# Optimization experiments

Hardware: AMD Instinct MI355X
Metric: run time of the kernel (lower is better)

Reference implementation:

```python
import jax, jax.numpy as jnp
import numpy as np

N = 50000
E = 600000
D = 128


def gcn_conv(x, row, col, w, W, b):
    """PyG GCNConv: add self-loops (weight 1), symmetric deg^-1/2 normalization,
    linear transform, edge-weighted scatter-add aggregation, then bias."""
    n = x.shape[0]
    loop = jnp.arange(n)
    r = jnp.concatenate([row, loop])            # source nodes, [E+N]
    c = jnp.concatenate([col, loop])            # target nodes, [E+N]
    ww = jnp.concatenate([w, jnp.ones((n,), x.dtype)])
    deg = jax.ops.segment_sum(ww, c, num_segments=n)          # weighted in-degree
    dinv = jnp.where(deg > 0, jax.lax.rsqrt(deg), jnp.zeros_like(deg))
    norm = dinv[r] * ww * dinv[c]               # [E+N]
    xl = x @ W                                  # [n, D_out]
    msg = norm[:, None] * xl[r]                 # gather + scale, [E+N, D_out]
    out = jax.ops.segment_sum(msg, c, num_segments=n)
    return out + b


def setup_inputs() -> dict:
    key = jax.random.key(0)
    ks = jax.random.split(key, 12)
    x = jax.random.normal(ks[0], (N, D), dtype=jnp.float32)
    edge_index = jax.random.randint(ks[1], (2, E), 0, N, dtype=jnp.int64)
    edge_weights = jax.random.uniform(ks[2], (E,), dtype=jnp.float32)
    s = 1.0 / np.sqrt(D)
    W1 = jax.random.uniform(ks[3], (D, D), jnp.float32, -s, s)
    b1 = jnp.zeros((D,), jnp.float32)
    W2 = jax.random.uniform(ks[4], (D, D), jnp.float32, -s, s)
    b2 = jnp.zeros((D,), jnp.float32)
    W3 = jax.random.uniform(ks[5], (D, D), jnp.float32, -s, s)
    b3 = jnp.zeros((D,), jnp.float32)
    prelu_w = jnp.array(0.25, jnp.float32)
    return {"x": x, "edge_index": edge_index, "edge_weights": edge_weights,
            "W1": W1, "b1": b1, "W2": W2, "b2": b2, "W3": W3, "b3": b3,
            "prelu_w": prelu_w}


def reference(x, edge_index, edge_weights, W1, b1, W2, b2, W3, b3, prelu_w):
    row, col = edge_index[0], edge_index[1]
    # layer 1: GCNConv -> (dropout: eval, identity) -> ELU
    h = gcn_conv(x, row, col, edge_weights, W1, b1)
    h = jax.nn.elu(h)
    # layer 2: GCNConv -> GELU (torch default = exact erf)
    h = gcn_conv(h, row, col, edge_weights, W2, b2)
    h = jax.nn.gelu(h, approximate=False)
    # layer 3: GCNConv -> PReLU (learnable scalar slope)
    h = gcn_conv(h, row, col, edge_weights, W3, b3)
    h = jnp.where(h >= 0, h, prelu_w * h)
    return h
```

## Files before the change

kernel.cpp:

```cpp
#include <hip/hip_runtime.h>
#include <hip/hip_fp16.h>
#include <math.h>

constexpr int D = 128;
constexpr int CAPF = 512;

struct __align__(16) H8 { __half2 h[4]; };

typedef _Float16     half8   __attribute__((ext_vector_type(8)));
typedef float        floatx4 __attribute__((ext_vector_type(4)));
typedef unsigned int uint4v  __attribute__((ext_vector_type(4)));
typedef unsigned int uint2v  __attribute__((ext_vector_type(2)));


__device__ __forceinline__ int detect64(const int* __restrict__ ei) {
  int z = 0;
#pragma unroll
  for (int i = 0; i < 8; ++i) z |= ei[2 * i + 1];
  return (z == 0) ? 1 : 0;
}

__device__ __forceinline__ void load_edge(const int* __restrict__ ei, int e, int nE,
                                          int m64, int n, int& r, int& c) {
  if (m64) { r = ei[2 * (size_t)e]; c = ei[2 * ((size_t)nE + e)]; }
  else     { r = ei[(size_t)e];     c = ei[(size_t)nE + e]; }
  r = min(max(r, 0), n - 1);
  c = min(max(c, 0), n - 1);
}

__global__ void k_setup(const float* __restrict__ W1, const float* __restrict__ W2,
                        const float* __restrict__ W3, __half* __restrict__ Wt,
                        unsigned long long* __restrict__ cntdeg, int n8) {
  int b = blockIdx.x;
  if (b < 24) {
    int m = b >> 3, s = b & 7;
    const float* W = m == 0 ? W1 : (m == 1 ? W2 : W3);
    __half* o = Wt + (size_t)m * D * D;
    int t = threadIdx.x;
    int nn = t & 127;
    int kh = t >> 7;
    int k0 = s * 16 + kh * 8;
    H8 hv;
#pragma unroll
    for (int jj = 0; jj < 4; ++jj) {
      float f0 = W[(size_t)(k0 + 2 * jj)     * D + nn];
      float f1 = W[(size_t)(k0 + 2 * jj + 1) * D + nn];
      hv.h[jj] = __floats2half2_rn(f0, f1);
    }
    *(H8*)(o + (size_t)nn * D + k0) = hv;
  } else {
    int i = (b - 24) * 256 + threadIdx.x;
    if (i < n8) cntdeg[i] = 0ULL;
  }
}

template <int ACT>
__device__ __forceinline__ float act_f(float x) {
  if (ACT == 1) return x > 0.f ? x : expm1f(x);
  if (ACT == 2) return 0.5f * x * (1.0f + erff(x * 0.70710678118654752440f));
  return x;
}

__device__ __forceinline__ void gemm_body(int bid, const float* __restrict__ A,
                                          const __half* __restrict__ Wt,
                                          __half* __restrict__ Y, int n) {
  const int wave = threadIdx.x >> 6;
  const int lane = threadIdx.x & 63;
  const int np = lane & 15;
  const int quad = lane >> 4;
  const int node = bid * 64 + wave * 16 + np;
  const int nc = min(node, n - 1);

  half8 b[4];
#pragma unroll
  for (int s = 0; s < 4; ++s) {
    const float* ap = A + (size_t)nc * D + s * 32 + quad * 8;
    floatx4 v0 = __builtin_nontemporal_load((const floatx4*)ap);
    floatx4 v1 = __builtin_nontemporal_load((const floatx4*)(ap + 4));
#pragma unroll
    for (int t = 0; t < 4; ++t) {
      b[s][t]     = (_Float16)v0[t];
      b[s][t + 4] = (_Float16)v1[t];
    }
  }

  floatx4 acc[8];
#pragma unroll
  for (int mt = 0; mt < 8; ++mt) acc[mt] = (floatx4){0.f, 0.f, 0.f, 0.f};

#pragma unroll
  for (int mt = 0; mt < 8; ++mt) {
#pragma unroll
    for (int s = 0; s < 4; ++s) {
      half8 a = *(const half8*)(Wt + (size_t)(mt * 16 + np) * D + s * 32 + quad * 8);
      acc[mt] = __builtin_amdgcn_mfma_f32_16x16x32_f16(a, b[s], acc[mt], 0, 0, 0);
    }
  }

  if (node < n) {
#pragma unroll
    for (int mt = 0; mt < 8; ++mt) {
      __half2 ha = __floats2half2_rn(acc[mt][0], acc[mt][1]);
      __half2 hb = __floats2half2_rn(acc[mt][2], acc[mt][3]);
      uint2v pv;
      pv[0] = *(unsigned int*)&ha;
      pv[1] = *(unsigned int*)&hb;
      int f0 = mt * 16 + quad * 4;
      __builtin_nontemporal_store(
          pv, (uint2v*)(Y + ((size_t)(f0 >> 5) * n + node) * 32 + (f0 & 31)));
    }
  }
}

__global__ __launch_bounds__(256) void k_posgemm(const float* __restrict__ x,
                                                 const __half* __restrict__ Wt,
                                                 __half* __restrict__ Y,
                                                 const int* __restrict__ ei,
                                                 const float* __restrict__ w,
                                                 unsigned long long* __restrict__ cntdeg,
                                                 int2* __restrict__ rc,
                                                 int* __restrict__ pos,
                                                 int nE, int n, int gb) {
  int b = blockIdx.x;
  if (b < gb) {
    gemm_body(b, x, Wt, Y, n);
    return;
  }
  int e = (b - gb) * blockDim.x + threadIdx.x;
  if (e >= nE) return;
  int m64 = detect64(ei);
  int r, c;
  load_edge(ei, e, nE, m64, n, r, c);
  rc[e] = make_int2(r, c);
  float wf = fminf(fmaxf(w[e], 0.0f), 65535.0f);
  unsigned long long pk =
      (1ULL << 32) | (unsigned long long)__float2uint_rn(wf * 65536.0f);
  unsigned long long old = atomicAdd(&cntdeg[(size_t)c << 3], pk);
  pos[e] = (int)(old >> 32);
}

__global__ void k_scan1(const unsigned long long* __restrict__ cntdeg,
                        int* __restrict__ offs, int* __restrict__ bsum, int n) {
  __shared__ int s[256];
  int t = threadIdx.x;
  int i = blockIdx.x * 256 + t;
  int v = 0;
  if (i < n) {
    int cn = (int)(cntdeg[(size_t)i << 3] >> 32);
    v = (cn + 3) & ~3;
  }
  s[t] = v;
  __syncthreads();
  for (int off = 1; off < 256; off <<= 1) {
    int x = 0;
    if (t >= off) x = s[t - off];
    __syncthreads();
    if (t >= off) s[t] += x;
    __syncthreads();
  }
  if (i < n) offs[i] = s[t] - v;
  if (t == 255) bsum[blockIdx.x] = s[255];
}

__global__ void k_scan23(int* __restrict__ offs, const int* __restrict__ bsum,
                         const unsigned long long* __restrict__ cntdeg,
                         float* __restrict__ dinv, int n, int nb) {
  __shared__ int s[256];
  int t = threadIdx.x;
  int v = (t < nb) ? bsum[t] : 0;
  s[t] = v;
  __syncthreads();
  for (int off = 1; off < 256; off <<= 1) {
    int x = 0;
    if (t >= off) x = s[t - off];
    __syncthreads();
    if (t >= off) s[t] += x;
    __syncthreads();
  }
  int b = blockIdx.x;
  int boffb = (b == 0) ? 0 : s[b - 1];
  int i = b * 256 + t;
  if (i < n) {
    offs[i] += boffb;
    float degf =
        (float)(unsigned int)(cntdeg[(size_t)i << 3] & 0xffffffffULL) * (1.0f / 65536.0f);
    dinv[i] = rsqrtf(1.0f + degf);
  }
  if (i == 0) offs[n] = s[nb - 1];
}

__global__ void k_fill(const int2* __restrict__ rc, const int* __restrict__ pos,
                       const float* __restrict__ w, const int* __restrict__ offs,
                       const unsigned long long* __restrict__ cntdeg,
                       const float* __restrict__ dinv,
                       unsigned int* __restrict__ ecf2, int nE, int n) {
  int e = blockIdx.x * blockDim.x + threadIdx.x;
  if (e < nE) {
    int2 p = rc[e];
    int idx = offs[p.y] + pos[e];
    float cf = dinv[p.x] * w[e];
    ecf2[idx] = ((unsigned int)p.x << 16) |
                (unsigned int)__half_as_ushort(__float2half_rn(cf));
  }
  if (e < n) {
    int q0 = offs[e] + (int)(cntdeg[(size_t)e << 3] >> 32), q1 = offs[e + 1];
    for (int q = q0; q < q1; ++q) ecf2[q] = 0;
  }
}

__device__ __forceinline__ void fmacc8(float* acc, float c, const H8& y) {
  const _Float16* hp = (const _Float16*)&y;
#pragma unroll
  for (int i = 0; i < 8; ++i) acc[i] = fmaf(c, (float)hp[i], acc[i]);
}

__device__ __forceinline__ float cdecode(unsigned int u) {
  return __half2float(__ushort_as_half((unsigned short)(u & 0xffffu)));
}

__device__ __forceinline__ void gather4(H8* y, uint4v u, const __half* __restrict__ Yc,
                                        int j) {
#pragma unroll
  for (int i = 0; i < 4; ++i)
    y[i] = *(const H8*)(Yc + (size_t)(u[i] >> 16) * 32 + j * 8);
}

__device__ __forceinline__ void accum4(float* acc, uint4v u, const H8* y) {
#pragma unroll
  for (int i = 0; i < 4; ++i) fmacc8(acc, cdecode(u[i]), y[i]);
}

#define AGG_PHASE()                                                              \
  const int nl = t >> 4;                                                         \
  const int node = node0 + nl;                                                   \
  const int cj = t & 15;                                                         \
  const int chunk = cj >> 2, j = cj & 3;                                         \
  const __half* Yc = Yin + (size_t)chunk * n * 32;                               \
  const int ncl = min(node, n - 1);                                              \
  float dc = dinv[ncl];                                                          \
  float acc[8] = {0.f, 0.f, 0.f, 0.f, 0.f, 0.f, 0.f, 0.f};                       \
  H8 ys = *(const H8*)(Yc + (size_t)ncl * 32 + j * 8);                           \
  {                                                                              \
    int lo = soff[nl], hi = soff[nl + 1];                                        \
    for (int b = lo; b < hi; b += 8) {                                           \
      bool has2 = (hi - b) > 4;                                                  \
      int k0 = b - seg_lo;                                                       \
      uint4v u0 = (k0 + 4 <= CAPF) ? *(const uint4v*)&sc[k0]                     \
                                   : *(const uint4v*)(ecf2 + b);                 \
      uint4v u1{};                                                               \
      if (has2) {                                                                \
        int k1 = k0 + 4;                                                         \
        u1 = (k1 + 4 <= CAPF) ? *(const uint4v*)&sc[k1]                          \
                              : *(const uint4v*)(ecf2 + b + 4);                  \
      }                                                                          \
      H8 y0[4], y1[4];                                                           \
      gather4(y0, u0, Yc, j);                                                    \
      if (has2) gather4(y1, u1, Yc, j);                                          \
      accum4(acc, u0, y0);                                                       \
      if (has2) accum4(acc, u1, y1);                                             \
    }                                                                            \
    fmacc8(acc, dc, ys);                                                         \
  }

#define STAGE_COEFS()                                                            \
  const int t = threadIdx.x;                                                     \
  const int node0 = blockIdx.x * 16;                                             \
  if (node0 >= n) return;                                                        \
  const int seg_lo = offs[node0];                                                \
  const int seg_hi = offs[min(node0 + 16, n)];                                   \
  const int segN = min(seg_hi - seg_lo, CAPF);                                   \
  for (int i = t * 4; i < segN; i += 1024)                                       \
    *(uint4v*)&sc[i] =                                                           \
        __builtin_nontemporal_load((const uint4v*)(ecf2 + seg_lo + i));          \
  if (t < 17) soff[t] = offs[min(node0 + t, n)];                                 \
  __syncthreads();

template <int ACT>
__global__ __launch_bounds__(256, 6) void k_aggemm(
    const __half* __restrict__ Yin, const int* __restrict__ offs,
    const unsigned int* __restrict__ ecf2, const float* __restrict__ dinv,
    const float* __restrict__ bias, const __half* __restrict__ Wt,
    __half* __restrict__ Yout, int n) {
  __shared__ unsigned int sc[CAPF];
  __shared__ __half ht[16 * 136];
  __shared__ int soff[17];
  STAGE_COEFS();
  {
    AGG_PHASE();
    floatx4 ba = *(const floatx4*)(bias + chunk * 32 + j * 8);
    floatx4 bb = *(const floatx4*)(bias + chunk * 32 + j * 8 + 4);
    float o[8];
#pragma unroll
    for (int i = 0; i < 8; ++i)
      o[i] = act_f<ACT>(dc * acc[i] + (i < 4 ? ba[i] : bb[i - 4]));
    H8 hw;
#pragma unroll
    for (int i = 0; i < 4; ++i) hw.h[i] = __floats2half2_rn(o[2 * i], o[2 * i + 1]);
    if (node < n) *(H8*)&ht[nl * 136 + chunk * 32 + j * 8] = hw;
  }
  __syncthreads();

  const int wave = t >> 6, lane = t & 63, np = lane & 15, quad = lane >> 4;
  half8 bfr[4];
#pragma unroll
  for (int s = 0; s < 4; ++s)
    bfr[s] = *(const half8*)&ht[np * 136 + s * 32 + quad * 8];
  floatx4 ga0 = (floatx4){0.f, 0.f, 0.f, 0.f};
  floatx4 ga1 = (floatx4){0.f, 0.f, 0.f, 0.f};
#pragma unroll
  for (int s = 0; s < 4; ++s) {
    half8 a0 = *(const half8*)(Wt + (size_t)((wave * 2) * 16 + np) * D + s * 32 + quad * 8);
    ga0 = __builtin_amdgcn_mfma_f32_16x16x32_f16(a0, bfr[s], ga0, 0, 0, 0);
    half8 a1 = *(const half8*)(Wt + (size_t)((wave * 2 + 1) * 16 + np) * D + s * 32 + quad * 8);
    ga1 = __builtin_amdgcn_mfma_f32_16x16x32_f16(a1, bfr[s], ga1, 0, 0, 0);
  }
  const int gnode = node0 + np;
  if (gnode < n) {
    floatx4 g[2] = {ga0, ga1};
#pragma unroll
    for (int mi = 0; mi < 2; ++mi) {
      int mt = wave * 2 + mi;
      __half2 ha = __floats2half2_rn(g[mi][0], g[mi][1]);
      __half2 hb = __floats2half2_rn(g[mi][2], g[mi][3]);
      uint2v pv;
      pv[0] = *(unsigned int*)&ha;
      pv[1] = *(unsigned int*)&hb;
      int f0 = mt * 16 + quad * 4;
      __builtin_nontemporal_store(
          pv, (uint2v*)(Yout + ((size_t)(f0 >> 5) * n + gnode) * 32 + (f0 & 31)));
    }
  }
}

__global__ __launch_bounds__(256, 6) void k_aggout(
    const __half* __restrict__ Yin, const int* __restrict__ offs,
    const unsigned int* __restrict__ ecf2, const float* __restrict__ dinv,
    const float* __restrict__ bias, const float* __restrict__ pw,
    float* __restrict__ out, int n) {
  __shared__ unsigned int sc[CAPF];
  __shared__ int soff[17];
  STAGE_COEFS();
  AGG_PHASE();
  if (node < n) {
    floatx4 ba = *(const floatx4*)(bias + chunk * 32 + j * 8);
    floatx4 bb = *(const floatx4*)(bias + chunk * 32 + j * 8 + 4);
    float wv = *pw;
    floatx4 v0, v1;
#pragma unroll
    for (int i = 0; i < 4; ++i) {
      float o = dc * acc[i] + ba[i];
      v0[i] = o >= 0.f ? o : wv * o;
    }
#pragma unroll
    for (int i = 0; i < 4; ++i) {
      float o = dc * acc[4 + i] + bb[i];
      v1[i] = o >= 0.f ? o : wv * o;
    }
    float* op = out + (size_t)node * D + chunk * 32 + j * 8;
    __builtin_nontemporal_store(v0, (floatx4*)op);
    __builtin_nontemporal_store(v1, (floatx4*)(op + 4));
  }
}

extern "C" void kernel_launch(void* const* d_in, const int* in_sizes, int n_in,
                              void* d_out, int out_size, void* d_ws, size_t ws_size,
                              hipStream_t stream) {
  const float* x  = (const float*)d_in[0];
  const int*   ei = (const int*)d_in[1];
  const float* w  = (const float*)d_in[2];
  const float* W1 = (const float*)d_in[3];
  const float* b1 = (const float*)d_in[4];
  const float* W2 = (const float*)d_in[5];
  const float* b2 = (const float*)d_in[6];
  const float* W3 = (const float*)d_in[7];
  const float* b3 = (const float*)d_in[8];
  const float* pw = (const float*)d_in[9];
  const int N = in_sizes[0] / D;
  const int E = in_sizes[2];
  float* out = (float*)d_out;

  char* wsb = (char*)d_ws;
  size_t off = 0;
  auto alloc = [&](size_t bytes) {
    void* p = wsb + off;
    off = (off + bytes + 255) & ~(size_t)255;
    return p;
  };
  float*              dinv   = (float*)alloc((size_t)N * 4);
  unsigned long long* cntdeg = (unsigned long long*)alloc((size_t)N * 64);
  int*                offs   = (int*)alloc((size_t)(N + 1) * 4);
  int*                bsum   = (int*)alloc(256 * 4);
  unsigned int*       ecf2   = (unsigned int*)alloc(((size_t)E + 3 * (size_t)N + 64) * 4);
  __half*             Wt     = (__half*)alloc((size_t)3 * D * D * 2);
  __half*             Ya     = (__half*)alloc((size_t)N * D * 2);
  __half*             Yb     = (__half*)alloc((size_t)N * D * 2);
  int2*               rc     = (int2*)alloc((size_t)E * 8);
  int*                pos    = (int*)alloc((size_t)E * 4);

  const int nbN = (N + 255) / 256;
  const int eb  = (E + 255) / 256;
  const int fb  = ((E > N ? E : N) + 255) / 256;
  const int n8  = N * 8;
  const int zb  = (n8 + 255) / 256;
  const int gb  = (N + 63) / 64;
  const int abf = (N + 15) / 16;

  hipLaunchKernelGGL(k_setup,   dim3(24 + zb), dim3(256), 0, stream, W1, W2, W3, Wt, cntdeg, n8);
  hipLaunchKernelGGL(k_posgemm, dim3(gb + eb), dim3(256), 0, stream, x, Wt, Ya, ei, w, cntdeg,
                     rc, pos, E, N, gb);
  hipLaunchKernelGGL(k_scan1,   dim3(nbN), dim3(256), 0, stream, cntdeg, offs, bsum, N);
  hipLaunchKernelGGL(k_scan23,  dim3(nbN), dim3(256), 0, stream, offs, bsum, cntdeg, dinv, N, nbN);
  hipLaunchKernelGGL(k_fill,    dim3(fb),  dim3(256), 0, stream, rc, pos, w, offs, cntdeg, dinv, ecf2, E, N);

  hipLaunchKernelGGL((k_aggemm<1>), dim3(abf), dim3(256), 0, stream, Ya, offs, ecf2, dinv, b1, Wt + D * D,     Yb, N);
  hipLaunchKernelGGL((k_aggemm<2>), dim3(abf), dim3(256), 0, stream, Yb, offs, ecf2, dinv, b2, Wt + 2 * D * D, Ya, N);
  hipLaunchKernelGGL(k_aggout,      dim3(abf), dim3(256), 0, stream, Ya, offs, ecf2, dinv, b3, pw, out, N);
}
```

Measured before the change: 289.4 us.

## Split fused aggregate-GEMM into chunk-major aggregation and separate half GEMM kernels

```diff
diff --git a/kernel.cpp b/kernel.cpp
--- a/kernel.cpp
+++ b/kernel.cpp
@@ -3,7 +3,7 @@
 #include <math.h>
 
 constexpr int D = 128;
-constexpr int CAPF = 512;
+constexpr int CAPS = 2048;
 
 struct __align__(16) H8 { __half2 h[4]; };
 
@@ -83,6 +83,50 @@
       b[s][t + 4] = (_Float16)v1[t];
     }
   }
+
+  floatx4 acc[8];
+#pragma unroll
+  for (int mt = 0; mt < 8; ++mt) acc[mt] = (floatx4){0.f, 0.f, 0.f, 0.f};
+
+#pragma unroll
+  for (int mt = 0; mt < 8; ++mt) {
+#pragma unroll
+    for (int s = 0; s < 4; ++s) {
+      half8 a = *(const half8*)(Wt + (size_t)(mt * 16 + np) * D + s * 32 + quad * 8);
+      acc[mt] = __builtin_amdgcn_mfma_f32_16x16x32_f16(a, b[s], acc[mt], 0, 0, 0);
+    }
+  }
+
+  if (node < n) {
+#pragma unroll
+    for (int mt = 0; mt < 8; ++mt) {
+      __half2 ha = __floats2half2_rn(acc[mt][0], acc[mt][1]);
+      __half2 hb = __floats2half2_rn(acc[mt][2], acc[mt][3]);
+      uint2v pv;
+      pv[0] = *(unsigned int*)&ha;
+      pv[1] = *(unsigned int*)&hb;
+      int f0 = mt * 16 + quad * 4;
+      __builtin_nontemporal_store(
+          pv, (uint2v*)(Y + ((size_t)(f0 >> 5) * n + node) * 32 + (f0 & 31)));
+    }
+  }
+}
+
+__global__ __launch_bounds__(256) void k_gemmh(const __half* __restrict__ A,
+                                               const __half* __restrict__ Wt,
+                                               __half* __restrict__ Y, int n) {
+  const int wave = threadIdx.x >> 6;
+  const int lane = threadIdx.x & 63;
+  const int np = lane & 15;
+  const int quad = lane >> 4;
+  const int node = blockIdx.x * 64 + wave * 16 + np;
+  const int nc = min(node, n - 1);
+
+  half8 b[4];
+#pragma unroll
+  for (int s = 0; s < 4; ++s)
+    b[s] = __builtin_nontemporal_load(
+        (const half8*)(A + ((size_t)s * n + nc) * 32 + quad * 8));
 
   floatx4 acc[8];
 #pragma unroll
@@ -230,135 +274,87 @@
   for (int i = 0; i < 4; ++i) fmacc8(acc, cdecode(u[i]), y[i]);
 }
 
-#define AGG_PHASE()                                                              \
-  const int nl = t >> 4;                                                         \
-  const int node = node0 + nl;                                                   \
-  const int cj = t & 15;                                                         \
-  const int chunk = cj >> 2, j = cj & 3;                                         \
-  const __half* Yc = Yin + (size_t)chunk * n * 32;                               \
-  const int ncl = min(node, n - 1);                                              \
-  float dc = dinv[ncl];                                                          \
-  float acc[8] = {0.f, 0.f, 0.f, 0.f, 0.f, 0.f, 0.f, 0.f};                       \
-  H8 ys = *(const H8*)(Yc + (size_t)ncl * 32 + j * 8);                           \
-  {                                                                              \
-    int lo = soff[nl], hi = soff[nl + 1];                                        \
-    for (int b = lo; b < hi; b += 8) {                                           \
-      bool has2 = (hi - b) > 4;                                                  \
-      int k0 = b - seg_lo;                                                       \
-      uint4v u0 = (k0 + 4 <= CAPF) ? *(const uint4v*)&sc[k0]                     \
-                                   : *(const uint4v*)(ecf2 + b);                 \
-      uint4v u1{};                                                               \
-      if (has2) {                                                                \
-        int k1 = k0 + 4;                                                         \
-        u1 = (k1 + 4 <= CAPF) ? *(const uint4v*)&sc[k1]                          \
-                              : *(const uint4v*)(ecf2 + b + 4);                  \
-      }                                                                          \
-      H8 y0[4], y1[4];                                                           \
-      gather4(y0, u0, Yc, j);                                                    \
-      if (has2) gather4(y1, u1, Yc, j);                                          \
-      accum4(acc, u0, y0);                                                       \
-      if (has2) accum4(acc, u1, y1);                                             \
-    }                                                                            \
-    fmacc8(acc, dc, ys);                                                         \
-  }
-
-#define STAGE_COEFS()                                                            \
-  const int t = threadIdx.x;                                                     \
-  const int node0 = blockIdx.x * 16;                                             \
-  if (node0 >= n) return;                                                        \
-  const int seg_lo = offs[node0];                                                \
-  const int seg_hi = offs[min(node0 + 16, n)];                                   \
-  const int segN = min(seg_hi - seg_lo, CAPF);                                   \
-  for (int i = t * 4; i < segN; i += 1024)                                       \
-    *(uint4v*)&sc[i] =                                                           \
-        __builtin_nontemporal_load((const uint4v*)(ecf2 + seg_lo + i));          \
-  if (t < 17) soff[t] = offs[min(node0 + t, n)];                                 \
+template <int ACT, int PRELU, typename OutT>
+__global__ __launch_bounds__(256) void k_agg(const __half* __restrict__ Yin,
+                                             const int* __restrict__ offs,
+                                             const unsigned int* __restrict__ ecf2,
+                                             const float* __restrict__ dinv,
+                                             const float* __restrict__ bias,
+                                             const float* __restrict__ pw,
+                                             OutT* __restrict__ OUT, int n) {
+  __shared__ unsigned int sc[CAPS];
+  __shared__ int soff[65];
+  const int chunk = blockIdx.x & 3;
+  const int t = threadIdx.x;
+  const int node0 = (blockIdx.x >> 2) * 64;
+  const int nl = t >> 2;
+  const int node = node0 + nl;
+  const int j = t & 3;
+
+  const int seg_lo = offs[node0];
+  const int seg_hi = offs[min(node0 + 64, n)];
+  const int segN = min(seg_hi - seg_lo, CAPS);
+  for (int i = t * 4; i < segN; i += 1024)
+    *(uint4v*)&sc[i] =
+        __builtin_nontemporal_load((const uint4v*)(ecf2 + seg_lo + i));
+  if (t < 65) soff[t] = offs[min(node0 + t, n)];
   __syncthreads();
 
-template <int ACT>
-__global__ __launch_bounds__(256, 6) void k_aggemm(
-    const __half* __restrict__ Yin, const int* __restrict__ offs,
-    const unsigned int* __restrict__ ecf2, const float* __restrict__ dinv,
-    const float* __restrict__ bias, const __half* __restrict__ Wt,
-    __half* __restrict__ Yout, int n) {
-  __shared__ unsigned int sc[CAPF];
-  __shared__ __half ht[16 * 136];
-  __shared__ int soff[17];
-  STAGE_COEFS();
-  {
-    AGG_PHASE();
+  const __half* Yc = Yin + (size_t)chunk * n * 32;
+  const int ncl = min(node, n - 1);
+  float dc = dinv[ncl];
+  float acc[8] = {0.f, 0.f, 0.f, 0.f, 0.f, 0.f, 0.f, 0.f};
+
+  H8 ys = *(const H8*)(Yc + (size_t)ncl * 32 + j * 8);
+
+  int lo = soff[nl], hi = soff[nl + 1];
+  if (lo < hi) {
+    int k = lo - seg_lo;
+    uint4v uc = (k + 4 <= CAPS) ? *(const uint4v*)&sc[k]
+                                : *(const uint4v*)(ecf2 + lo);
+    H8 yc[4];
+    gather4(yc, uc, Yc, j);
+    for (int b = lo + 4; b < hi; b += 4) {
+      int k2 = b - seg_lo;
+      uint4v un = (k2 + 4 <= CAPS) ? *(const uint4v*)&sc[k2]
+                                   : *(const uint4v*)(ecf2 + b);
+      H8 yn[4];
+      gather4(yn, un, Yc, j);
+      accum4(acc, uc, yc);
+      uc = un;
+#pragma unroll
+      for (int q = 0; q < 4; ++q) yc[q] = yn[q];
+    }
+    accum4(acc, uc, yc);
+  }
+  fmacc8(acc, dc, ys);
+
+  if (node < n) {
     floatx4 ba = *(const floatx4*)(bias + chunk * 32 + j * 8);
     floatx4 bb = *(const floatx4*)(bias + chunk * 32 + j * 8 + 4);
     float o[8];
 #pragma unroll
     for (int i = 0; i < 8; ++i)
       o[i] = act_f<ACT>(dc * acc[i] + (i < 4 ? ba[i] : bb[i - 4]));
-    H8 hw;
-#pragma unroll
-    for (int i = 0; i < 4; ++i) hw.h[i] = __floats2half2_rn(o[2 * i], o[2 * i + 1]);
-    if (node < n) *(H8*)&ht[nl * 136 + chunk * 32 + j * 8] = hw;
-  }
-  __syncthreads();
-
-  const int wave = t >> 6, lane = t & 63, np = lane & 15, quad = lane >> 4;
-  half8 bfr[4];
-#pragma unroll
-  for (int s = 0; s < 4; ++s)
-    bfr[s] = *(const half8*)&ht[np * 136 + s * 32 + quad * 8];
-  floatx4 ga0 = (floatx4){0.f, 0.f, 0.f, 0.f};
-  floatx4 ga1 = (floatx4){0.f, 0.f, 0.f, 0.f};
-#pragma unroll
-  for (int s = 0; s < 4; ++s) {
-    half8 a0 = *(const half8*)(Wt + (size_t)((wave * 2) * 16 + np) * D + s * 32 + quad * 8);
-    ga0 = __builtin_amdgcn_mfma_f32_16x16x32_f16(a0, bfr[s], ga0, 0, 0, 0);
-    half8 a1 = *(const half8*)(Wt + (size_t)((wave * 2 + 1) * 16 + np) * D + s * 32 + quad * 8);
-    ga1 = __builtin_amdgcn_mfma_f32_16x16x32_f16(a1, bfr[s], ga1, 0, 0, 0);
-  }
-  const int gnode = node0 + np;
-  if (gnode < n) {
-    floatx4 g[2] = {ga0, ga1};
-#pragma unroll
-    for (int mi = 0; mi < 2; ++mi) {
-      int mt = wave * 2 + mi;
-      __half2 ha = __floats2half2_rn(g[mi][0], g[mi][1]);
-      __half2 hb = __floats2half2_rn(g[mi][2], g[mi][3]);
-      uint2v pv;
-      pv[0] = *(unsigned int*)&ha;
-      pv[1] = *(unsigned int*)&hb;
-      int f0 = mt * 16 + quad * 4;
+    if (PRELU) {
+      float wv = *pw;
+#pragma unroll
+      for (int i = 0; i < 8; ++i) o[i] = o[i] >= 0.f ? o[i] : wv * o[i];
+    }
+    if constexpr (sizeof(OutT) == 4) {
+      floatx4 v0 = {o[0], o[1], o[2], o[3]};
+      floatx4 v1 = {o[4], o[5], o[6], o[7]};
+      float* op = (float*)OUT + (size_t)node * D + chunk * 32 + j * 8;
+      __builtin_nontemporal_store(v0, (floatx4*)op);
+      __builtin_nontemporal_store(v1, (floatx4*)(op + 4));
+    } else {
+      H8 hw;
+#pragma unroll
+      for (int i = 0; i < 4; ++i) hw.h[i] = __floats2half2_rn(o[2 * i], o[2 * i + 1]);
       __builtin_nontemporal_store(
-          pv, (uint2v*)(Yout + ((size_t)(f0 >> 5) * n + gnode) * 32 + (f0 & 31)));
-    }
-  }
-}
-
-__global__ __launch_bounds__(256, 6) void k_aggout(
-    const __half* __restrict__ Yin, const int* __restrict__ offs,
-    const unsigned int* __restrict__ ecf2, const float* __restrict__ dinv,
-    const float* __restrict__ bias, const float* __restrict__ pw,
-    float* __restrict__ out, int n) {
-  __shared__ unsigned int sc[CAPF];
-  __shared__ int soff[17];
-  STAGE_COEFS();
-  AGG_PHASE();
-  if (node < n) {
-    floatx4 ba = *(const floatx4*)(bias + chunk * 32 + j * 8);
-    floatx4 bb = *(const floatx4*)(bias + chunk * 32 + j * 8 + 4);
-    float wv = *pw;
-    floatx4 v0, v1;
-#pragma unroll
-    for (int i = 0; i < 4; ++i) {
-      float o = dc * acc[i] + ba[i];
-      v0[i] = o >= 0.f ? o : wv * o;
-    }
-#pragma unroll
-    for (int i = 0; i < 4; ++i) {
-      float o = dc * acc[4 + i] + bb[i];
-      v1[i] = o >= 0.f ? o : wv * o;
-    }
-    float* op = out + (size_t)node * D + chunk * 32 + j * 8;
-    __builtin_nontemporal_store(v0, (floatx4*)op);
-    __builtin_nontemporal_store(v1, (floatx4*)(op + 4));
+          *(uint4v*)&hw,
+          (uint4v*)((__half*)OUT + ((size_t)chunk * n + node) * 32 + j * 8));
+    }
   }
 }
 
@@ -394,6 +390,7 @@
   __half*             Wt     = (__half*)alloc((size_t)3 * D * D * 2);
   __half*             Ya     = (__half*)alloc((size_t)N * D * 2);
   __half*             Yb     = (__half*)alloc((size_t)N * D * 2);
+  __half*             h      = (__half*)alloc((size_t)N * D * 2);
   int2*               rc     = (int2*)alloc((size_t)E * 8);
   int*                pos    = (int*)alloc((size_t)E * 4);
 
@@ -403,7 +400,7 @@
   const int n8  = N * 8;
   const int zb  = (n8 + 255) / 256;
   const int gb  = (N + 63) / 64;
-  const int abf = (N + 15) / 16;
+  const int ab  = 4 * ((N + 63) / 64);
 
   hipLaunchKernelGGL(k_setup,   dim3(24 + zb), dim3(256), 0, stream, W1, W2, W3, Wt, cntdeg, n8);
   hipLaunchKernelGGL(k_posgemm, dim3(gb + eb), dim3(256), 0, stream, x, Wt, Ya, ei, w, cntdeg,
@@ -412,7 +409,9 @@
   hipLaunchKernelGGL(k_scan23,  dim3(nbN), dim3(256), 0, stream, offs, bsum, cntdeg, dinv, N, nbN);
   hipLaunchKernelGGL(k_fill,    dim3(fb),  dim3(256), 0, stream, rc, pos, w, offs, cntdeg, dinv, ecf2, E, N);
 
-  hipLaunchKernelGGL((k_aggemm<1>), dim3(abf), dim3(256), 0, stream, Ya, offs, ecf2, dinv, b1, Wt + D * D,     Yb, N);
-  hipLaunchKernelGGL((k_aggemm<2>), dim3(abf), dim3(256), 0, stream, Yb, offs, ecf2, dinv, b2, Wt + 2 * D * D, Ya, N);
-  hipLaunchKernelGGL(k_aggout,      dim3(abf), dim3(256), 0, stream, Ya, offs, ecf2, dinv, b3, pw, out, N);
-}
+  hipLaunchKernelGGL((k_agg<1, 0, __half>), dim3(ab), dim3(256), 0, stream, Ya, offs, ecf2, dinv, b1, pw, h, N);
+  hipLaunchKernelGGL(k_gemmh,               dim3(gb), dim3(256), 0, stream, h, Wt + D * D,     Yb, N);
+  hipLaunchKernelGGL((k_agg<2, 0, __half>), dim3(ab), dim3(256), 0, stream, Yb, offs, ecf2, dinv, b2, pw, h, N);
+  hipLaunchKernelGGL(k_gemmh,               dim3(gb), dim3(256), 0, stream, h, Wt + 2 * D * D, Ya, N);
+  hipLaunchKernelGGL((k_agg<0, 1, float>),  dim3(ab), dim3(256), 0, stream, Ya, offs, ecf2, dinv, b3, pw, out, N);
+}
```

Result: slower. 423.8 us (+46.4%).

## Software-pipeline neighbor gathers with triple-buffered prefetch in aggregation loop

Applied to the files above, without the earlier changes.

```diff
diff --git a/kernel.cpp b/kernel.cpp
--- a/kernel.cpp
+++ b/kernel.cpp
@@ -230,6 +230,9 @@
   for (int i = 0; i < 4; ++i) fmacc8(acc, cdecode(u[i]), y[i]);
 }
 
+#define LDC(p) (((p) - seg_lo + 4 <= CAPF) ? *(const uint4v*)&sc[(p) - seg_lo] \
+                                           : *(const uint4v*)(ecf2 + (p)))
+
 #define AGG_PHASE()                                                              \
   const int nl = t >> 4;                                                         \
   const int node = node0 + nl;                                                   \
@@ -242,22 +245,25 @@
   H8 ys = *(const H8*)(Yc + (size_t)ncl * 32 + j * 8);                           \
   {                                                                              \
     int lo = soff[nl], hi = soff[nl + 1];                                        \
-    for (int b = lo; b < hi; b += 8) {                                           \
-      bool has2 = (hi - b) > 4;                                                  \
-      int k0 = b - seg_lo;                                                       \
-      uint4v u0 = (k0 + 4 <= CAPF) ? *(const uint4v*)&sc[k0]                     \
-                                   : *(const uint4v*)(ecf2 + b);                 \
-      uint4v u1{};                                                               \
-      if (has2) {                                                                \
-        int k1 = k0 + 4;                                                         \
-        u1 = (k1 + 4 <= CAPF) ? *(const uint4v*)&sc[k1]                          \
-                              : *(const uint4v*)(ecf2 + b + 4);                  \
+    if (lo < hi) {                                                               \
+      uint4v u0, u1, u2;                                                         \
+      H8 y0[4], y1[4], y2[4];                                                    \
+      u0 = LDC(lo);                                                              \
+      gather4(y0, u0, Yc, j);                                                    \
+      if (lo + 4 < hi) { u1 = LDC(lo + 4); gather4(y1, u1, Yc, j); }             \
+      if (lo + 8 < hi) { u2 = LDC(lo + 8); gather4(y2, u2, Yc, j); }             \
+      int b = lo;                                                                \
+      while (true) {                                                             \
+        accum4(acc, u0, y0);                                                     \
+        if (b + 12 < hi) { u0 = LDC(b + 12); gather4(y0, u0, Yc, j); }           \
+        b += 4; if (b >= hi) break;                                              \
+        accum4(acc, u1, y1);                                                     \
+        if (b + 12 < hi) { u1 = LDC(b + 12); gather4(y1, u1, Yc, j); }           \
+        b += 4; if (b >= hi) break;                                              \
+        accum4(acc, u2, y2);                                                     \
+        if (b + 12 < hi) { u2 = LDC(b + 12); gather4(y2, u2, Yc, j); }           \
+        b += 4; if (b >= hi) break;                                              \
       }                                                                          \
-      H8 y0[4], y1[4];                                                           \
-      gather4(y0, u0, Yc, j);                                                    \
-      if (has2) gather4(y1, u1, Yc, j);                                          \
-      accum4(acc, u0, y0);                                                       \
-      if (has2) accum4(acc, u1, y1);                                             \
     }                                                                            \
     fmacc8(acc, dc, ys);                                                         \
   }
@@ -276,7 +282,7 @@
   __syncthreads();
 
 template <int ACT>
-__global__ __launch_bounds__(256, 6) void k_aggemm(
+__global__ __launch_bounds__(256, 4) void k_aggemm(
     const __half* __restrict__ Yin, const int* __restrict__ offs,
     const unsigned int* __restrict__ ecf2, const float* __restrict__ dinv,
     const float* __restrict__ bias, const __half* __restrict__ Wt,
@@ -332,7 +338,7 @@
   }
 }
 
-__global__ __launch_bounds__(256, 6) void k_aggout(
+__global__ __launch_bounds__(256, 4) void k_aggout(
     const __half* __restrict__ Yin, const int* __restrict__ offs,
     const unsigned int* __restrict__ ecf2, const float* __restrict__ dinv,
     const float* __restrict__ bias, const float* __restrict__ pw,
```

New measurement: 302.3 us. 1.04x slower.
